# Performance work log

Hardware: AMD Instinct MI355X
Metric: run time of the kernel (lower is better)

Reference implementation:

```python
import jax, jax.numpy as jnp
import numpy as np

B, SQ, SK, D = 32, 2048, 2048, 64


def setup_inputs() -> dict:
    key = jax.random.key(0)
    kq, kk, km = jax.random.split(key, 3)
    q = jax.random.normal(kq, (B, SQ, D), dtype=jnp.float32)
    k = jax.random.normal(kk, (B, SK, D), dtype=jnp.float32)
    mask = jax.random.randint(km, (B, SQ, SK), 0, 2, dtype=jnp.int32)
    return {"q": q, "k": k, "mask": mask}


def reference(q, k, mask):
    # scores = q @ k^T / sqrt(D)  -> [B, SQ, SK]
    scale = 1.0 / np.sqrt(q.shape[-1]).astype(np.float32)
    scores = jnp.einsum('bqd,bkd->bqk', q, k) * scale
    scores = jnp.where(mask == 0, -jnp.inf, scores)
    return jax.nn.softmax(scores, axis=-1)
```

## Files before the change

### kernel.cpp

```cpp
#include <hip/hip_runtime.h>
#include <math.h>

constexpr int BB  = 32;
constexpr int SQL = 2048;
constexpr int SKL = 2048;
constexpr int DD  = 64;

using f32x4 = __attribute__((ext_vector_type(4))) float;
using bfrag = __attribute__((ext_vector_type(8))) short;

static __device__ __forceinline__ unsigned short f2bf(float x) {
    unsigned u = __float_as_uint(x);
    u = u + 0x7FFFu + ((u >> 16) & 1u);
    return (unsigned short)(u >> 16);
}
static __device__ __forceinline__ float bf2f(unsigned short h) {
    return __uint_as_float((unsigned)h << 16);
}

static __device__ __forceinline__ void gld16(const void* g, void* l) {
    __builtin_amdgcn_global_load_lds(
        (const __attribute__((address_space(1))) void*)(size_t)g,
        (__attribute__((address_space(3))) void*)(unsigned)(size_t)l,
        16, 0, 0);
}

__global__ __launch_bounds__(256) void split_k_swz(
    const float* __restrict__ k, unsigned char* __restrict__ kswz)
{
    const int i0 = blockIdx.x * blockDim.x + threadIdx.x;
    const int g  = i0 & 7;
    const int c  = (i0 >> 3) & 2047;
    const int b  = i0 >> 14;
    const float* kp = k + ((size_t)(b * 2048 + c)) * DD + g * 8;
    bfrag h, lo;
    #pragma unroll
    for (int j = 0; j < 8; ++j) {
        const float x = kp[j];
        const unsigned short hh = f2bf(x);
        h[j]  = (short)hh;
        lo[j] = (short)f2bf(x - bf2f(hh));
    }
    const int sw = (c & 7) << 4;
    unsigned char* rec = kswz + ((size_t)(b * 2048 + c)) * 256;
    *(bfrag*)(rec + ((g * 16) ^ sw))       = h;
    *(bfrag*)(rec + 128 + ((g * 16) ^ sw)) = lo;
}

template<bool PRE>
__global__ __launch_bounds__(512, 4) void sdpa_v10(
    const float* __restrict__ q, const float* __restrict__ k,
    const int* __restrict__ mask, const unsigned char* __restrict__ kswz,
    float* __restrict__ out)
{
    __shared__ char pool[81920];

    const int t   = threadIdx.x;
    const int l   = t & 63;
    const int w   = t >> 6;
    const int lr  = l & 15;
    const int lg  = l >> 4;
    const int bid = blockIdx.x;
    const int swz = (bid & 7) * 512 + (bid >> 3);
    const int b   = swz >> 7;
    const int r0  = (swz & 127) * 16;
    const int c0  = w * 256;
    const size_t rowg = (size_t)b * SQL + (size_t)(r0 + lr);
    const int swk = (lr & 7) << 4;

    char* kseg = pool + w * 10240;
    char* mseg = kseg + 8192;

    constexpr float QS = 0.18033688011112042f;
    bfrag qh0, ql0, qh1, ql1;
    {
        const float* qp = q + rowg * DD + lg * 8;
        const f32x4 x0 = *reinterpret_cast<const f32x4*>(qp);
        const f32x4 x1 = *reinterpret_cast<const f32x4*>(qp + 4);
        const f32x4 y0 = *reinterpret_cast<const f32x4*>(qp + 32);
        const f32x4 y1 = *reinterpret_cast<const f32x4*>(qp + 36);
        #pragma unroll
        for (int j = 0; j < 4; ++j) {
            float a = x0[j] * QS, c = x1[j] * QS;
            float d = y0[j] * QS, e = y1[j] * QS;
            unsigned short h;
            h = f2bf(a); qh0[j]     = (short)h; ql0[j]     = (short)f2bf(a - bf2f(h));
            h = f2bf(c); qh0[j + 4] = (short)h; ql0[j + 4] = (short)f2bf(c - bf2f(h));
            h = f2bf(d); qh1[j]     = (short)h; ql1[j]     = (short)f2bf(d - bf2f(h));
            h = f2bf(e); qh1[j + 4] = (short)h; ql1[j + 4] = (short)f2bf(e - bf2f(h));
        }
    }

    const char* ksrc = PRE ? (const char*)(kswz + (size_t)b * SKL * 256) : nullptr;
    const float* kraw = PRE ? nullptr : k + (size_t)b * SKL * DD;

    const int* msrc = mask + ((size_t)b * SQL + (size_t)(r0 + (l >> 2))) * SKL
                           + c0 + (((l & 3) ^ ((l >> 3) & 3)) << 2);
    const int moff = lr * 64 + ((lg ^ ((lr >> 1) & 3)) << 4);
    const int* mrp = PRE ? nullptr : mask + rowg * SKL + c0 + lg * 4;

#define STAGE(T)                                                               \
    do {                                                                       \
        char* _kd = kseg + (((T) & 1) << 12);                                  \
        if constexpr (PRE) {                                                   \
            const char* _ks = ksrc + (size_t)(c0 + (T) * 16) * 256;            \
            gld16(_ks + l * 16,        _kd + l * 16);                          \
            gld16(_ks + 1024 + l * 16, _kd + 1024 + l * 16);                   \
            gld16(_ks + 2048 + l * 16, _kd + 2048 + l * 16);                   \
            gld16(_ks + 3072 + l * 16, _kd + 3072 + l * 16);                   \
            gld16(msrc + (T) * 16, mseg + (((T) & 1) << 10) + l * 16);         \
        } else {                                                               \
            const float* _kc = kraw + (size_t)(c0 + (T) * 16 + lr) * DD;       \
            const f32x4 _a0 = *(const f32x4*)(_kc + lg * 8);                   \
            const f32x4 _a1 = *(const f32x4*)(_kc + lg * 8 + 4);               \
            const f32x4 _b0 = *(const f32x4*)(_kc + (lg + 4) * 8);             \
            const f32x4 _b1 = *(const f32x4*)(_kc + (lg + 4) * 8 + 4);         \
            bfrag _h, _o;                                                      \
            _Pragma("unroll")                                                  \
            for (int _j = 0; _j < 4; ++_j) {                                   \
                unsigned short _t;                                             \
                _t = f2bf(_a0[_j]); _h[_j]   = (short)_t;                      \
                _o[_j]   = (short)f2bf(_a0[_j] - bf2f(_t));                    \
                _t = f2bf(_a1[_j]); _h[_j+4] = (short)_t;                      \
                _o[_j+4] = (short)f2bf(_a1[_j] - bf2f(_t));                    \
            }                                                                  \
            char* _rec = _kd + lr * 256;                                       \
            *(bfrag*)(_rec + ((lg * 16) ^ swk))       = _h;                    \
            *(bfrag*)(_rec + 128 + ((lg * 16) ^ swk)) = _o;                    \
            _Pragma("unroll")                                                  \
            for (int _j = 0; _j < 4; ++_j) {                                   \
                unsigned short _t;                                             \
                _t = f2bf(_b0[_j]); _h[_j]   = (short)_t;                      \
                _o[_j]   = (short)f2bf(_b0[_j] - bf2f(_t));                    \
                _t = f2bf(_b1[_j]); _h[_j+4] = (short)_t;                      \
                _o[_j+4] = (short)f2bf(_b1[_j] - bf2f(_t));                    \
            }                                                                  \
            *(bfrag*)(_rec + (((lg + 4) * 16) ^ swk))       = _h;              \
            *(bfrag*)(_rec + 128 + (((lg + 4) * 16) ^ swk)) = _o;              \
        }                                                                      \
    } while (0)

#define ITER(T, VMC)                                                           \
    do {                                                                       \
        if constexpr (PRE)                                                     \
            asm volatile("s_waitcnt vmcnt(" #VMC ")" ::: "memory");            \
        const char* _c = kseg + (((T) & 1) << 12) + lr * 256;                  \
        const bfrag _kh0 = *(const bfrag*)(_c + ((lg * 16) ^ swk));            \
        const bfrag _kh1 = *(const bfrag*)(_c + (((lg + 4) * 16) ^ swk));      \
        const bfrag _kl0 = *(const bfrag*)(_c + 128 + ((lg * 16) ^ swk));      \
        const bfrag _kl1 = *(const bfrag*)(_c + 128 + (((lg + 4) * 16) ^ swk));\
        int4 _mv;                                                              \
        if constexpr (PRE)                                                     \
            _mv = *(const int4*)(mseg + (((T) & 1) << 10) + moff);             \
        else                                                                   \
            _mv = *(const int4*)(mrp + (T) * 16);                              \
        asm volatile("s_waitcnt lgkmcnt(0)" ::: "memory");                     \
        __builtin_amdgcn_sched_barrier(0);                                     \
        if constexpr ((T) + 2 < 16) STAGE((T) + 2);                            \
        f32x4 _a1 = {0.f, 0.f, 0.f, 0.f};                                      \
        f32x4 _a2 = {0.f, 0.f, 0.f, 0.f};                                      \
        f32x4 _a3 = {0.f, 0.f, 0.f, 0.f};                                      \
        _a1 = __builtin_amdgcn_mfma_f32_16x16x32_bf16(_kl0, qh0, _a1, 0, 0, 0);\
        _a2 = __builtin_amdgcn_mfma_f32_16x16x32_bf16(_kh0, ql0, _a2, 0, 0, 0);\
        _a3 = __builtin_amdgcn_mfma_f32_16x16x32_bf16(_kh0, qh0, _a3, 0, 0, 0);\
        _a1 = __builtin_amdgcn_mfma_f32_16x16x32_bf16(_kl1, qh1, _a1, 0, 0, 0);\
        _a2 = __builtin_amdgcn_mfma_f32_16x16x32_bf16(_kh1, ql1, _a2, 0, 0, 0);\
        _a3 = __builtin_amdgcn_mfma_f32_16x16x32_bf16(_kh1, qh1, _a3, 0, 0, 0);\
        const f32x4 _s = (_a1 + _a2) + _a3;                                    \
        const float _e0 = (_mv.x != 0) ? exp2f(_s[0]) : 0.f;                   \
        const float _e1 = (_mv.y != 0) ? exp2f(_s[1]) : 0.f;                   \
        const float _e2 = (_mv.z != 0) ? exp2f(_s[2]) : 0.f;                   \
        const float _e3 = (_mv.w != 0) ? exp2f(_s[3]) : 0.f;                   \
        psum += (_e0 + _e1) + (_e2 + _e3);                                     \
        sc[2 * (T)    ] = (unsigned)f2bf(_e0) | ((unsigned)f2bf(_e1) << 16);   \
        sc[2 * (T) + 1] = (unsigned)f2bf(_e2) | ((unsigned)f2bf(_e3) << 16);   \
    } while (0)

    unsigned sc[32];
    float psum = 0.f;

    STAGE(0);
    STAGE(1);

    ITER(0,  5); ITER(1,  5); ITER(2,  5); ITER(3,  5);
    ITER(4,  5); ITER(5,  5); ITER(6,  5); ITER(7,  5);
    ITER(8,  5); ITER(9,  5); ITER(10, 5); ITER(11, 5);
    ITER(12, 5); ITER(13, 5); ITER(14, 5); ITER(15, 0);
#undef ITER
#undef STAGE

    float s = psum;
    s += __shfl_xor(s, 16, 64);
    s += __shfl_xor(s, 32, 64);

    __syncthreads();
    float* s_red = (float*)pool;
    if (l < 16) s_red[w * 16 + lr] = s;
    __syncthreads();

    float tot = 0.f;
    #pragma unroll
    for (int ww = 0; ww < 8; ++ww)
        tot += s_red[ww * 16 + lr];
    const float rinv = 1.0f / tot;

    float* op = out + rowg * SKL + c0 + lg * 4;
    #pragma unroll
    for (int T = 0; T < 16; ++T) {
        const unsigned p01 = sc[2 * T];
        const unsigned p23 = sc[2 * T + 1];
        f32x4 o;
        o[0] = bf2f((unsigned short)(p01 & 0xffffu)) * rinv;
        o[1] = bf2f((unsigned short)(p01 >> 16))     * rinv;
        o[2] = bf2f((unsigned short)(p23 & 0xffffu)) * rinv;
        o[3] = bf2f((unsigned short)(p23 >> 16))     * rinv;
        *reinterpret_cast<f32x4*>(op + T * 16) = o;
    }
}

extern "C" void kernel_launch(void* const* d_in, const int* in_sizes, int n_in,
                              void* d_out, int out_size, void* d_ws, size_t ws_size,
                              hipStream_t stream) {
    const float* q    = (const float*)d_in[0];
    const float* k    = (const float*)d_in[1];
    const int*   mask = (const int*)d_in[2];
    float*       out  = (float*)d_out;

    const size_t KS_B = (size_t)BB * SKL * 256;

    dim3 grid(4096);

    if (ws_size >= KS_B) {
        unsigned char* ksp = (unsigned char*)d_ws;
        split_k_swz<<<2048, 256, 0, stream>>>(k, ksp);
        sdpa_v10<true><<<grid, 512, 0, stream>>>(q, k, mask, ksp, out);
    } else {
        sdpa_v10<false><<<grid, 512, 0, stream>>>(q, k, mask, nullptr, out);
    }
}
```

Before: 352.5 us.

## Split each row tile across 16 waves with single-buffered LDS staging

Doubles the block to 1024 threads so each of 16 waves covers 128 key columns instead of 256. That halves per-wave register state (score cache) and LDS per wave, and the LDS ring drops from double to single buffering with a full vmcnt wait. It also issues the first stage before the Q conversion, merges the three MFMA accumulators into one chain, and packs bf16 with v_cvt_pk_bf16_f32. The aim is more resident waves to hide memory latency on the mask/output stream, at the cost of less prefetch depth and a serial MFMA dependency chain.

Result: slower. 395.1 us (+12.1%).

```diff
diff --git a/kernel.cpp b/kernel.cpp
--- a/kernel.cpp
+++ b/kernel.cpp
@@ -48,7 +48,7 @@
 }
 
 template<bool PRE>
-__global__ __launch_bounds__(512, 4) void sdpa_v10(
+__global__ __launch_bounds__(1024, 8) void sdpa_v11(
     const float* __restrict__ q, const float* __restrict__ k,
     const int* __restrict__ mask, const unsigned char* __restrict__ kswz,
     float* __restrict__ out)
@@ -64,12 +64,93 @@
     const int swz = (bid & 7) * 512 + (bid >> 3);
     const int b   = swz >> 7;
     const int r0  = (swz & 127) * 16;
-    const int c0  = w * 256;
+    const int c0  = w * 128;
     const size_t rowg = (size_t)b * SQL + (size_t)(r0 + lr);
     const int swk = (lr & 7) << 4;
 
-    char* kseg = pool + w * 10240;
-    char* mseg = kseg + 8192;
+    char* kseg = pool + w * 5120;
+    char* mseg = kseg + 4096;
+
+    const char* ksrc = PRE ? (const char*)(kswz + ((size_t)b * SKL + c0) * 256) : nullptr;
+    const float* kraw = PRE ? nullptr : k + (size_t)b * SKL * DD;
+    const int* msrc = mask + ((size_t)b * SQL + (size_t)(r0 + (l >> 2))) * SKL
+                           + c0 + (((l & 3) ^ ((l >> 3) & 3)) << 2);
+    const int moff = lr * 64 + ((lg ^ ((lr >> 1) & 3)) << 4);
+
+#define STAGE(T)                                                               \
+    do {                                                                       \
+        if constexpr (PRE) {                                                   \
+            const char* _ks = ksrc + (size_t)(T) * 4096;                       \
+            gld16(_ks + l * 16,        kseg + l * 16);                         \
+            gld16(_ks + 1024 + l * 16, kseg + 1024 + l * 16);                  \
+            gld16(_ks + 2048 + l * 16, kseg + 2048 + l * 16);                  \
+            gld16(_ks + 3072 + l * 16, kseg + 3072 + l * 16);                  \
+            gld16(msrc + (T) * 16, mseg + l * 16);                             \
+        } else {                                                               \
+            const float* _kc = kraw + (size_t)(c0 + (T) * 16 + lr) * DD;       \
+            const f32x4 _a0 = *(const f32x4*)(_kc + lg * 8);                   \
+            const f32x4 _a1 = *(const f32x4*)(_kc + lg * 8 + 4);               \
+            const f32x4 _b0 = *(const f32x4*)(_kc + (lg + 4) * 8);             \
+            const f32x4 _b1 = *(const f32x4*)(_kc + (lg + 4) * 8 + 4);         \
+            bfrag _h, _o;                                                      \
+            _Pragma("unroll")                                                  \
+            for (int _j = 0; _j < 4; ++_j) {                                   \
+                unsigned short _t2;                                            \
+                _t2 = f2bf(_a0[_j]); _h[_j]   = (short)_t2;                    \
+                _o[_j]   = (short)f2bf(_a0[_j] - bf2f(_t2));                   \
+                _t2 = f2bf(_a1[_j]); _h[_j+4] = (short)_t2;                    \
+                _o[_j+4] = (short)f2bf(_a1[_j] - bf2f(_t2));                   \
+            }                                                                  \
+            char* _rec = kseg + lr * 256;                                      \
+            *(bfrag*)(_rec + ((lg * 16) ^ swk))       = _h;                    \
+            *(bfrag*)(_rec + 128 + ((lg * 16) ^ swk)) = _o;                    \
+            _Pragma("unroll")                                                  \
+            for (int _j = 0; _j < 4; ++_j) {                                   \
+                unsigned short _t2;                                            \
+                _t2 = f2bf(_b0[_j]); _h[_j]   = (short)_t2;                    \
+                _o[_j]   = (short)f2bf(_b0[_j] - bf2f(_t2));                   \
+                _t2 = f2bf(_b1[_j]); _h[_j+4] = (short)_t2;                    \
+                _o[_j+4] = (short)f2bf(_b1[_j] - bf2f(_t2));                   \
+            }                                                                  \
+            *(bfrag*)(_rec + (((lg + 4) * 16) ^ swk))       = _h;              \
+            *(bfrag*)(_rec + 128 + (((lg + 4) * 16) ^ swk)) = _o;              \
+            const int4 _mv = *(const int4*)(msrc + (T) * 16);                  \
+            *(int4*)(mseg + l * 16) = _mv;                                     \
+        }                                                                      \
+    } while (0)
+
+#define ITER(T)                                                                \
+    do {                                                                       \
+        if constexpr (PRE)                                                     \
+            asm volatile("s_waitcnt vmcnt(0)" ::: "memory");                   \
+        const char* _c = kseg + lr * 256;                                      \
+        const bfrag _kh0 = *(const bfrag*)(_c + ((lg * 16) ^ swk));            \
+        const bfrag _kh1 = *(const bfrag*)(_c + (((lg + 4) * 16) ^ swk));      \
+        const bfrag _kl0 = *(const bfrag*)(_c + 128 + ((lg * 16) ^ swk));      \
+        const bfrag _kl1 = *(const bfrag*)(_c + 128 + (((lg + 4) * 16) ^ swk));\
+        const int4 _mv = *(const int4*)(mseg + moff);                          \
+        asm volatile("s_waitcnt lgkmcnt(0)" ::: "memory");                     \
+        __builtin_amdgcn_sched_barrier(0);                                     \
+        if constexpr ((T) + 1 < 8) STAGE((T) + 1);                             \
+        f32x4 _a = {0.f, 0.f, 0.f, 0.f};                                       \
+        _a = __builtin_amdgcn_mfma_f32_16x16x32_bf16(_kl0, qh0, _a, 0, 0, 0);  \
+        _a = __builtin_amdgcn_mfma_f32_16x16x32_bf16(_kh0, ql0, _a, 0, 0, 0);  \
+        _a = __builtin_amdgcn_mfma_f32_16x16x32_bf16(_kh0, qh0, _a, 0, 0, 0);  \
+        _a = __builtin_amdgcn_mfma_f32_16x16x32_bf16(_kl1, qh1, _a, 0, 0, 0);  \
+        _a = __builtin_amdgcn_mfma_f32_16x16x32_bf16(_kh1, ql1, _a, 0, 0, 0);  \
+        _a = __builtin_amdgcn_mfma_f32_16x16x32_bf16(_kh1, qh1, _a, 0, 0, 0);  \
+        const float _e0 = (_mv.x != 0) ? exp2f(_a[0]) : 0.f;                   \
+        const float _e1 = (_mv.y != 0) ? exp2f(_a[1]) : 0.f;                   \
+        const float _e2 = (_mv.z != 0) ? exp2f(_a[2]) : 0.f;                   \
+        const float _e3 = (_mv.w != 0) ? exp2f(_a[3]) : 0.f;                   \
+        psum += (_e0 + _e1) + (_e2 + _e3);                                     \
+        asm volatile("v_cvt_pk_bf16_f32 %0, %1, %2"                            \
+                     : "=v"(sc[2 * (T)]) : "v"(_e0), "v"(_e1));                \
+        asm volatile("v_cvt_pk_bf16_f32 %0, %1, %2"                            \
+                     : "=v"(sc[2 * (T) + 1]) : "v"(_e2), "v"(_e3));            \
+    } while (0)
+
+    STAGE(0);
 
     constexpr float QS = 0.18033688011112042f;
     bfrag qh0, ql0, qh1, ql1;
@@ -91,101 +172,11 @@
         }
     }
 
-    const char* ksrc = PRE ? (const char*)(kswz + (size_t)b * SKL * 256) : nullptr;
-    const float* kraw = PRE ? nullptr : k + (size_t)b * SKL * DD;
-
-    const int* msrc = mask + ((size_t)b * SQL + (size_t)(r0 + (l >> 2))) * SKL
-                           + c0 + (((l & 3) ^ ((l >> 3) & 3)) << 2);
-    const int moff = lr * 64 + ((lg ^ ((lr >> 1) & 3)) << 4);
-    const int* mrp = PRE ? nullptr : mask + rowg * SKL + c0 + lg * 4;
-
-#define STAGE(T)                                                               \
-    do {                                                                       \
-        char* _kd = kseg + (((T) & 1) << 12);                                  \
-        if constexpr (PRE) {                                                   \
-            const char* _ks = ksrc + (size_t)(c0 + (T) * 16) * 256;            \
-            gld16(_ks + l * 16,        _kd + l * 16);                          \
-            gld16(_ks + 1024 + l * 16, _kd + 1024 + l * 16);                   \
-            gld16(_ks + 2048 + l * 16, _kd + 2048 + l * 16);                   \
-            gld16(_ks + 3072 + l * 16, _kd + 3072 + l * 16);                   \
-            gld16(msrc + (T) * 16, mseg + (((T) & 1) << 10) + l * 16);         \
-        } else {                                                               \
-            const float* _kc = kraw + (size_t)(c0 + (T) * 16 + lr) * DD;       \
-            const f32x4 _a0 = *(const f32x4*)(_kc + lg * 8);                   \
-            const f32x4 _a1 = *(const f32x4*)(_kc + lg * 8 + 4);               \
-            const f32x4 _b0 = *(const f32x4*)(_kc + (lg + 4) * 8);             \
-            const f32x4 _b1 = *(const f32x4*)(_kc + (lg + 4) * 8 + 4);         \
-            bfrag _h, _o;                                                      \
-            _Pragma("unroll")                                                  \
-            for (int _j = 0; _j < 4; ++_j) {                                   \
-                unsigned short _t;                                             \
-                _t = f2bf(_a0[_j]); _h[_j]   = (short)_t;                      \
-                _o[_j]   = (short)f2bf(_a0[_j] - bf2f(_t));                    \
-                _t = f2bf(_a1[_j]); _h[_j+4] = (short)_t;                      \
-                _o[_j+4] = (short)f2bf(_a1[_j] - bf2f(_t));                    \
-            }                                                                  \
-            char* _rec = _kd + lr * 256;                                       \
-            *(bfrag*)(_rec + ((lg * 16) ^ swk))       = _h;                    \
-            *(bfrag*)(_rec + 128 + ((lg * 16) ^ swk)) = _o;                    \
-            _Pragma("unroll")                                                  \
-            for (int _j = 0; _j < 4; ++_j) {                                   \
-                unsigned short _t;                                             \
-                _t = f2bf(_b0[_j]); _h[_j]   = (short)_t;                      \
-                _o[_j]   = (short)f2bf(_b0[_j] - bf2f(_t));                    \
-                _t = f2bf(_b1[_j]); _h[_j+4] = (short)_t;                      \
-                _o[_j+4] = (short)f2bf(_b1[_j] - bf2f(_t));                    \
-            }                                                                  \
-            *(bfrag*)(_rec + (((lg + 4) * 16) ^ swk))       = _h;              \
-            *(bfrag*)(_rec + 128 + (((lg + 4) * 16) ^ swk)) = _o;              \
-        }                                                                      \
-    } while (0)
-
-#define ITER(T, VMC)                                                           \
-    do {                                                                       \
-        if constexpr (PRE)                                                     \
-            asm volatile("s_waitcnt vmcnt(" #VMC ")" ::: "memory");            \
-        const char* _c = kseg + (((T) & 1) << 12) + lr * 256;                  \
-        const bfrag _kh0 = *(const bfrag*)(_c + ((lg * 16) ^ swk));            \
-        const bfrag _kh1 = *(const bfrag*)(_c + (((lg + 4) * 16) ^ swk));      \
-        const bfrag _kl0 = *(const bfrag*)(_c + 128 + ((lg * 16) ^ swk));      \
-        const bfrag _kl1 = *(const bfrag*)(_c + 128 + (((lg + 4) * 16) ^ swk));\
-        int4 _mv;                                                              \
-        if constexpr (PRE)                                                     \
-            _mv = *(const int4*)(mseg + (((T) & 1) << 10) + moff);             \
-        else                                                                   \
-            _mv = *(const int4*)(mrp + (T) * 16);                              \
-        asm volatile("s_waitcnt lgkmcnt(0)" ::: "memory");                     \
-        __builtin_amdgcn_sched_barrier(0);                                     \
-        if constexpr ((T) + 2 < 16) STAGE((T) + 2);                            \
-        f32x4 _a1 = {0.f, 0.f, 0.f, 0.f};                                      \
-        f32x4 _a2 = {0.f, 0.f, 0.f, 0.f};                                      \
-        f32x4 _a3 = {0.f, 0.f, 0.f, 0.f};                                      \
-        _a1 = __builtin_amdgcn_mfma_f32_16x16x32_bf16(_kl0, qh0, _a1, 0, 0, 0);\
-        _a2 = __builtin_amdgcn_mfma_f32_16x16x32_bf16(_kh0, ql0, _a2, 0, 0, 0);\
-        _a3 = __builtin_amdgcn_mfma_f32_16x16x32_bf16(_kh0, qh0, _a3, 0, 0, 0);\
-        _a1 = __builtin_amdgcn_mfma_f32_16x16x32_bf16(_kl1, qh1, _a1, 0, 0, 0);\
-        _a2 = __builtin_amdgcn_mfma_f32_16x16x32_bf16(_kh1, ql1, _a2, 0, 0, 0);\
-        _a3 = __builtin_amdgcn_mfma_f32_16x16x32_bf16(_kh1, qh1, _a3, 0, 0, 0);\
-        const f32x4 _s = (_a1 + _a2) + _a3;                                    \
-        const float _e0 = (_mv.x != 0) ? exp2f(_s[0]) : 0.f;                   \
-        const float _e1 = (_mv.y != 0) ? exp2f(_s[1]) : 0.f;                   \
-        const float _e2 = (_mv.z != 0) ? exp2f(_s[2]) : 0.f;                   \
-        const float _e3 = (_mv.w != 0) ? exp2f(_s[3]) : 0.f;                   \
-        psum += (_e0 + _e1) + (_e2 + _e3);                                     \
-        sc[2 * (T)    ] = (unsigned)f2bf(_e0) | ((unsigned)f2bf(_e1) << 16);   \
-        sc[2 * (T) + 1] = (unsigned)f2bf(_e2) | ((unsigned)f2bf(_e3) << 16);   \
-    } while (0)
-
-    unsigned sc[32];
+    unsigned sc[16];
     float psum = 0.f;
 
-    STAGE(0);
-    STAGE(1);
-
-    ITER(0,  5); ITER(1,  5); ITER(2,  5); ITER(3,  5);
-    ITER(4,  5); ITER(5,  5); ITER(6,  5); ITER(7,  5);
-    ITER(8,  5); ITER(9,  5); ITER(10, 5); ITER(11, 5);
-    ITER(12, 5); ITER(13, 5); ITER(14, 5); ITER(15, 0);
+    ITER(0); ITER(1); ITER(2); ITER(3);
+    ITER(4); ITER(5); ITER(6); ITER(7);
 #undef ITER
 #undef STAGE
 
@@ -200,13 +191,13 @@
 
     float tot = 0.f;
     #pragma unroll
-    for (int ww = 0; ww < 8; ++ww)
+    for (int ww = 0; ww < 16; ++ww)
         tot += s_red[ww * 16 + lr];
     const float rinv = 1.0f / tot;
 
     float* op = out + rowg * SKL + c0 + lg * 4;
     #pragma unroll
-    for (int T = 0; T < 16; ++T) {
+    for (int T = 0; T < 8; ++T) {
         const unsigned p01 = sc[2 * T];
         const unsigned p23 = sc[2 * T + 1];
         f32x4 o;
@@ -233,8 +224,8 @@
     if (ws_size >= KS_B) {
         unsigned char* ksp = (unsigned char*)d_ws;
         split_k_swz<<<2048, 256, 0, stream>>>(k, ksp);
-        sdpa_v10<true><<<grid, 512, 0, stream>>>(q, k, mask, ksp, out);
+        sdpa_v11<true><<<grid, 1024, 0, stream>>>(q, k, mask, ksp, out);
     } else {
-        sdpa_v10<false><<<grid, 512, 0, stream>>>(q, k, mask, nullptr, out);
-    }
-}
+        sdpa_v11<false><<<grid, 1024, 0, stream>>>(q, k, mask, nullptr, out);
+    }
+}
```
